# Kernel tuning notes

Measured on AMD Instinct MI355X. Metric: run time of the kernel, lower is better.

## Reference

```python
import jax, jax.numpy as jnp
import numpy as np
jax.config.update("jax_enable_x64", True)

MS_H = 10
MS_W = 10
EPS = 1e-8


def _window_mean(x, kh, kw):
    # x: [B, H, W]; VALID avg-pool with kernel (kh, kw), stride 1, via integral image
    c = jnp.cumsum(jnp.cumsum(x, axis=1), axis=2)
    c = jnp.pad(c, ((0, 0), (1, 0), (1, 0)))
    H, W = x.shape[1], x.shape[2]
    oh, ow = H - kh + 1, W - kw + 1
    s = (c[:, kh:kh + oh, kw:kw + ow] - c[:, :oh, kw:kw + ow]
         - c[:, kh:kh + oh, :ow] + c[:, :oh, :ow])
    return s / (kh * kw)


def _translate_bilinear(imgs, dy, dx):
    # imgs: [B, H, W]; out[b,i,j] = imgs[b, i - dy[b], j - dx[b]] (bilinear, zero fill)
    B, H, W = imgs.shape
    yq = jnp.arange(H, dtype=imgs.dtype)[None, :, None] - dy[:, None, None]
    xq = jnp.arange(W, dtype=imgs.dtype)[None, None, :] - dx[:, None, None]
    y0 = jnp.floor(yq); x0 = jnp.floor(xq)
    wy = yq - y0;       wx = xq - x0
    y0i = y0.astype(jnp.int32); x0i = x0.astype(jnp.int32)
    b = jnp.arange(B)[:, None, None]
    def samp(yi, xi):
        valid = (yi >= 0) & (yi < H) & (xi >= 0) & (xi < W)
        v = imgs[b, jnp.clip(yi, 0, H - 1), jnp.clip(xi, 0, W - 1)]
        return jnp.where(valid, v, jnp.zeros((), imgs.dtype))
    v00 = samp(y0i, x0i);     v01 = samp(y0i, x0i + 1)
    v10 = samp(y0i + 1, x0i); v11 = samp(y0i + 1, x0i + 1)
    return (v00 * (1 - wy) * (1 - wx) + v01 * (1 - wy) * wx
            + v10 * wy * (1 - wx) + v11 * wy * wx)


def _motion_correct(fr, template):
    # fr: [1, B, H, W, 1] float32; template: [H, W] float32
    B = fr.shape[1]
    H, W = template.shape
    mx, my = H // 2, W // 2
    # --- template normalization ---
    t_zm = template - jnp.mean(template)
    t_var = jnp.sum(jnp.square(t_zm)) + EPS
    target_freq = jnp.fft.fft2(t_zm.astype(jnp.complex128))            # [H, W]
    imgs = fr[0, :, :, :, 0]                                           # [B, H, W]
    imgs_zm = imgs - jnp.mean(imgs, axis=(1, 2), keepdims=True)
    # --- local statistics (avg_pool2d VALID, kernel = template minus shift margins) ---
    kh, kw = H - 2 * MS_W, W - 2 * MS_H
    m1 = _window_mean(imgs, kh, kw)                                    # [B, 2mw+1, 2mh+1]
    m2 = _window_mean(jnp.square(imgs), kh, kw)
    imgs_var = m2 - jnp.square(m1) / (kh * kw) + EPS
    imgs_var = jnp.where(imgs_var < 0, 0.0, imgs_var)
    denominator = jnp.sqrt(t_var * imgs_var)
    # --- FFT cross-correlation (fft3d over batch+spatial, exactly as the TF code) ---
    fr_freq = jnp.fft.fftn(imgs_zm.astype(jnp.complex128), axes=(0, 1, 2))
    img_product = fr_freq * jnp.conj(target_freq)[None]
    cc = jnp.abs(jnp.fft.ifftn(img_product, axes=(0, 1, 2))).astype(jnp.float32)
    rolled = jnp.roll(cc, (B, mx, my), axis=(0, 1, 2))
    nom = rolled[:, mx - MS_W:mx + MS_W + 1, my - MS_H:my + MS_H + 1]
    ncc = nom / denominator
    ncc = jnp.where(jnp.isnan(ncc), 0.0, ncc)                          # [B, 2mw+1, 2mh+1]
    # --- integer peak ---
    flat = ncc.reshape(B, -1)
    am = jnp.argmax(flat, axis=1)
    shx = am // (2 * MS_H + 1)
    shy = am % (2 * MS_H + 1)
    sh_x_n = -(shx - MS_H).astype(jnp.float32)
    sh_y_n = -(shy - MS_W).astype(jnp.float32)
    # --- log-parabolic sub-pixel refinement ---
    l = jnp.log(ncc)
    b = jnp.arange(B)
    lxm1 = l[b, shx - 1, shy]; lxp1 = l[b, shx + 1, shy]
    lym1 = l[b, shx, shy - 1]; lyp1 = l[b, shx, shy + 1]
    lc4 = 4.0 * l[b, shx, shy]
    sh_x_n = sh_x_n - (lxm1 - lxp1) / (2 * lxm1 - lc4 + 2 * lxp1)
    sh_y_n = sh_y_n - (lym1 - lyp1) / (2 * lym1 - lc4 + 2 * lyp1)
    # --- bilinear translate; tfa translations = [sh_y (dx, width), sh_x (dy, height)] ---
    warped = _translate_bilinear(imgs, sh_x_n, sh_y_n)                 # [B, H, W]
    return jnp.transpose(warped, (0, 2, 1)).reshape(B, H * W)


def setup_inputs() -> dict:
    H = W = 512
    B = 32
    k1, k2, k3 = jax.random.split(jax.random.key(0), 3)
    # smooth (low-pass) random template so the NCC peak is smooth/positive around its max
    noise = jax.random.normal(k1, (H, W))
    f = jnp.sqrt(jnp.fft.fftfreq(H)[:, None] ** 2 + jnp.fft.fftfreq(W)[None, :] ** 2)
    lp = (f < 0.05).astype(jnp.complex128)
    template = jnp.real(jnp.fft.ifft2(jnp.fft.fft2(noise) * lp))
    template = (template / template.std()).astype(jnp.float32)
    # frames: template shifted by small random integer offsets + noise
    shifts = jax.random.randint(k2, (B, 2), -5, 6)
    frames = jax.vmap(lambda s: jnp.roll(template, (s[0], s[1]), axis=(0, 1)))(shifts)
    frames = frames + 0.05 * jax.random.normal(k3, (B, H, W), dtype=jnp.float32)
    fr = frames[None, :, :, :, None].astype(jnp.float32)
    return {"fr": fr, "template": template}


def reference(fr, template):
    return _motion_correct(fr, template)
```

## Files before the change

kernel.cpp:

```cpp
#include <hip/hip_runtime.h>
#include <math.h>

#define HH 512
#define WW 512
#define NPIX (HH*WW)
#define NB 32
#define NS 21
#define KWIN 492
#define NKB 256
#define MT28 28
#define PARTSZ (MT28*32*16)

typedef __attribute__((ext_vector_type(8))) short short8;
typedef __attribute__((ext_vector_type(8))) unsigned short ushort8;
typedef __attribute__((ext_vector_type(4))) float floatx4;

__device__ __forceinline__ unsigned short f2bf(float f) {
    unsigned u = __float_as_uint(f);
    unsigned r = (u + 0x7fffu + ((u >> 16) & 1u)) >> 16;
    return (unsigned short)r;
}

__global__ __launch_bounds__(256) void stage1(
    const float* __restrict__ fr, const float* __restrict__ tpl,
    unsigned short* __restrict__ frBi, unsigned short* __restrict__ tplv,
    float* __restrict__ I1, float* __restrict__ I2,
    double* __restrict__ sum1, double* __restrict__ sum2)
{
    __shared__ unsigned short tile[64][136];
    int blk = blockIdx.x;
    int t   = threadIdx.x;
    if (blk < 512) {
        int kbase   = blk * 512;
        int kc8base = blk * 64;
        int sub  = t >> 7;
        int tq   = t & 127;
        int kc8l = tq >> 1;
        int j4   = (tq & 1) * 4;
#pragma unroll
        for (int h = 0; h < 2; ++h) {
#pragma unroll
            for (int n2 = 0; n2 < 16; n2 += 2) {
                int nl = n2 + sub;
                const float* src = fr + (size_t)(h * 16 + nl) * NPIX + kbase + tq * 4;
                float4 v = *(const float4*)src;
                unsigned short* d = &tile[kc8l][nl * 8 + j4];
                d[0] = f2bf(v.x); d[1] = f2bf(v.y); d[2] = f2bf(v.z); d[3] = f2bf(v.w);
            }
            __syncthreads();
            for (int c = t; c < 1024; c += 256) {
                int kl = c >> 4;
                int nl = c & 15;
                ushort8 o = *(ushort8*)&tile[kl][nl * 8];
                *(ushort8*)(frBi + ((size_t)(kc8base + kl) * 32 + h * 16 + nl) * 8) = o;
            }
            __syncthreads();
        }
    } else if (blk < 1024) {
        int id = blk - 512;
        int b  = id >> 4;
        int yg = id & 15;
        int y0, ny;
        if (yg < 8) { y0 = 20 + 30 * yg; ny = 30; }
        else        { y0 = 260 + 29 * (yg - 8); ny = 29; }
        const float* img = fr + (size_t)b * NPIX;
        int xa = t, xb = t + 256;
        float s1a = 0.f, s2a = 0.f, s1b = 0.f, s2b = 0.f;
        for (int y = y0; y < y0 + ny; ++y) {
            float va = img[(size_t)y * WW + xa];
            float vb = img[(size_t)y * WW + xb];
            s1a += va; s2a += va * va;
            s1b += vb; s2b += vb * vb;
        }
        atomicAdd(&I1[b * WW + xa], s1a); atomicAdd(&I2[b * WW + xa], s2a);
        atomicAdd(&I1[b * WW + xb], s1b); atomicAdd(&I2[b * WW + xb], s2b);
    } else if (blk < 1032) {
        int gq = blk - 1024;
        int y0 = 64 * gq;
        int xa = t, xb = t + 256;
        float s1a = 0.f, s2a = 0.f, s1b = 0.f, s2b = 0.f;
        for (int y = y0; y < y0 + 64; ++y) {
            float va = tpl[(size_t)y * WW + xa];
            float vb = tpl[(size_t)y * WW + xb];
            s1a += va; s2a += va * va;
            s1b += vb; s2b += vb * vb;
        }
        double d1 = (double)s1a + (double)s1b;
        double d2 = (double)s2a + (double)s2b;
        for (int off = 32; off; off >>= 1) {
            d1 += __shfl_down(d1, off);
            d2 += __shfl_down(d2, off);
        }
        __shared__ double r1[4], r2[4];
        int lane = t & 63, wv = t >> 6;
        if (lane == 0) { r1[wv] = d1; r2[wv] = d2; }
        __syncthreads();
        if (t == 0) {
            atomicAdd(&sum1[32], r1[0] + r1[1] + r1[2] + r1[3]);
            atomicAdd(&sum2[32], r2[0] + r2[1] + r2[2] + r2[3]);
        }
    } else {
        int blk2 = blk - 1032;
        int dv   = blk2 / 34;
        int prg  = blk2 % 34;
        int prEnd = min(16 * prg + 16, 532);
        for (int pr = 16 * prg; pr < prEnd; ++pr) {
            int sy = (pr + 502) & 511;
            const float* srow = tpl + (size_t)sy * WW;
            unsigned short* drow = tplv + ((size_t)dv * 532 + pr) * 512;
            for (int x = t; x < 512; x += 256) {
                int sx = (x - dv + 522) & 511;
                drow[x] = f2bf(srow[sx]);
            }
        }
    }
}

__global__ __launch_bounds__(448) void corr_mfma(
    const unsigned short* __restrict__ frBi,
    const unsigned short* __restrict__ tplv,
    float* __restrict__ part)
{
    const int l    = threadIdx.x & 63;
    const int mg2  = threadIdx.x >> 6;
    const int half = blockIdx.x & 1;
    const int idx  = blockIdx.x >> 1;
    const int kb   = ((idx & 7) << 5) | (idx >> 3);
    const int k0   = kb << 10;
    const int kg   = l >> 4;
    const int ln   = l & 15;
    const int tp   = 7 * half + mg2;

    const unsigned short* pA[2];
#pragma unroll
    for (int mt = 0; mt < 2; ++mt) {
        int m_g = 32 * tp + 16 * mt + ln;
        int du  = (m_g * 1561) >> 15;
        int dv  = m_g - 21 * du;
        if (m_g >= 441) { du = 0; dv = 0; }
        pA[mt] = tplv + ((size_t)(dv * 532 + 20 - du) * 512 + 8 * kg + k0);
    }
    const unsigned short* pB0 = frBi + ((size_t)k0 * 32 + kg * 256 + ln * 8);
    const unsigned short* pB1 = pB0 + 128;

    floatx4 acc00 = {}, acc01 = {}, acc10 = {}, acc11 = {};

#pragma unroll
    for (int ks = 0; ks < 32; ++ks) {
        short8 A0 = *(const short8*)pA[0];
        short8 A1 = *(const short8*)pA[1];
        short8 B0 = *(const short8*)pB0;
        short8 B1 = *(const short8*)pB1;
        acc00 = __builtin_amdgcn_mfma_f32_16x16x32_bf16(A0, B0, acc00, 0, 0, 0);
        acc01 = __builtin_amdgcn_mfma_f32_16x16x32_bf16(A0, B1, acc01, 0, 0, 0);
        acc10 = __builtin_amdgcn_mfma_f32_16x16x32_bf16(A1, B0, acc10, 0, 0, 0);
        acc11 = __builtin_amdgcn_mfma_f32_16x16x32_bf16(A1, B1, acc11, 0, 0, 0);
        pA[0] += 32; pA[1] += 32; pB0 += 1024; pB1 += 1024;
    }

    {
        size_t base = ((size_t)kb * MT28 + 2 * tp) * 32;
        floatx4* p;
        p = (floatx4*)(part + (base + ln)      * 16 + 4 * kg); *p = acc00;
        p = (floatx4*)(part + (base + 16 + ln) * 16 + 4 * kg); *p = acc01;
        p = (floatx4*)(part + (base + 32 + ln) * 16 + 4 * kg); *p = acc10;
        p = (floatx4*)(part + (base + 48 + ln) * 16 + 4 * kg); *p = acc11;
    }
}

__global__ __launch_bounds__(512) void reduce_stage2(
    const float* __restrict__ part, float* __restrict__ cc,
    const float* __restrict__ fr, const float* __restrict__ I1,
    const float* __restrict__ I2, double* __restrict__ sum1,
    const double* __restrict__ sum2, float* __restrict__ denom)
{
    __shared__ double wr1[NS][8], wr2[NS][8], wrT[8];
    __shared__ float  e1[NS][40], e2[NS][40];
    __shared__ double totals1[NS], totals2[NS];

    int blk = blockIdx.x;
    if (blk < 224) {
        int oct = blk / 28;
        int j   = (blk % 28) * 512 + threadIdx.x;
        const float* p = part + (size_t)(oct * 32) * PARTSZ + j;
        float s = 0.f;
#pragma unroll 8
        for (int i = 0; i < 32; ++i)
            s += p[(size_t)i * PARTSZ];
        int mr    = j & 15;
        int n     = (j >> 4) & 31;
        int mtile = j >> 9;
        int m = mtile * 16 + mr;
        if (m < 441)
            atomicAdd(&cc[(size_t)n * 441 + m], s);
        return;
    }

    int b = blk - 224;
    int x = threadIdx.x;
    const float* img = fr + (size_t)b * NPIX;
    float top[20], bot[20];
#pragma unroll
    for (int y = 0; y < 20; ++y) top[y] = img[(size_t)y * WW + x];
#pragma unroll
    for (int y = 0; y < 20; ++y) bot[y] = img[(size_t)(492 + y) * WW + x];

    float t1 = 0.f, t2 = 0.f, b1 = 0.f, b2 = 0.f;
#pragma unroll
    for (int y = 0; y < 20; ++y) {
        t1 += top[y]; t2 += top[y] * top[y];
        b1 += bot[y]; b2 += bot[y] * bot[y];
    }
    float i1 = I1[b * WW + x], i2 = I2[b * WW + x];
    int lane = x & 63, wv = x >> 6;

    double tot = (double)i1 + (double)t1 + (double)b1;
    for (int off = 32; off; off >>= 1) tot += __shfl_down(tot, off);
    if (lane == 0) wrT[wv] = tot;

    float s1 = i1 + t1, s2 = i2 + t2;
#pragma unroll
    for (int u = 0; u < NS; ++u) {
        if (u) {
            float a = top[u-1], c = bot[u-1];
            s1 += c - a;
            s2 += c * c - a * a;
        }
        double d1 = (double)s1, d2 = (double)s2;
        for (int off = 32; off; off >>= 1) {
            d1 += __shfl_down(d1, off);
            d2 += __shfl_down(d2, off);
        }
        if (lane == 0) { wr1[u][wv] = d1; wr2[u][wv] = d2; }
        if (x < 20)        { e1[u][x]       = s1; e2[u][x]       = s2; }
        else if (x >= 492) { e1[u][x - 472] = s1; e2[u][x - 472] = s2; }
    }
    __syncthreads();
    if (x == 0) {
        double s = 0.0;
        for (int i = 0; i < 8; ++i) s += wrT[i];
        sum1[b] = s;
    }
    if (x < NS) {
        double a = 0.0, c = 0.0;
        for (int i = 0; i < 8; ++i) { a += wr1[x][i]; c += wr2[x][i]; }
        totals1[x] = a; totals2[x] = c;
    }
    __syncthreads();
    if (x < NS * NS) {
        int u = x / NS, v = x - NS * u;
        double S1 = totals1[u], S2 = totals2[u];
        for (int j = 0; j < v; ++j)  { S1 -= (double)e1[u][j];      S2 -= (double)e2[u][j]; }
        for (int j = v; j < 20; ++j) { S1 -= (double)e1[u][20 + j]; S2 -= (double)e2[u][20 + j]; }
        const double inv = 1.0 / ((double)KWIN * (double)KWIN);
        double m1 = S1 * inv, m2 = S2 * inv;
        double var = m2 - (m1 * m1) * inv + 1e-8;
        if (var < 0.0) var = 0.0;
        double tv = sum2[32] - sum1[32] * sum1[32] * (1.0 / (double)NPIX) + 1e-8;
        denom[(size_t)b * NS * NS + x] = (float)sqrt(tv * var);
    }
}

__global__ __launch_bounds__(64) void argmax_kernel(
    const float* __restrict__ cc, const float* __restrict__ denom,
    const double* __restrict__ sum1, float* __restrict__ shifts)
{
    int b = blockIdx.x;
    const float* C = cc    + (size_t)b * NS * NS;
    const float* D = denom + (size_t)b * NS * NS;
    float corr = (float)(sum1[b] * sum1[32] * (1.0 / (double)NPIX));
    int l = threadIdx.x;
    float best = -1e30f; int bidx = NS * NS;
    for (int i = l; i < NS * NS; i += 64) {
        float v = fabsf(C[i] - corr) / D[i];
        if (v != v) v = 0.f;
        if (v > best) { best = v; bidx = i; }
    }
    for (int off = 32; off; off >>= 1) {
        float ov = __shfl_down(best, off);
        int   oi = __shfl_down(bidx, off);
        if (ov > best || (ov == best && oi < bidx)) { best = ov; bidx = oi; }
    }
    if (l == 0) {
        int shx = bidx / NS, shy = bidx % NS;
        auto nccAt = [&](int i, int j) -> float {
            i = (i < 0) ? i + NS : i; i = (i > NS - 1) ? NS - 1 : i;
            j = (j < 0) ? j + NS : j; j = (j > NS - 1) ? NS - 1 : j;
            float v = fabsf(C[i * NS + j] - corr) / D[i * NS + j];
            if (v != v) v = 0.f;
            return v;
        };
        float lc  = logf(nccAt(shx, shy));
        float lxm = logf(nccAt(shx - 1, shy));
        float lxp = logf(nccAt(shx + 1, shy));
        float lym = logf(nccAt(shx, shy - 1));
        float lyp = logf(nccAt(shx, shy + 1));
        float shxn = -(float)(shx - 10) - (lxm - lxp) / (2.f * lxm - 4.f * lc + 2.f * lxp);
        float shyn = -(float)(shy - 10) - (lym - lyp) / (2.f * lym - 4.f * lc + 2.f * lyp);
        shifts[b]      = shxn;
        shifts[32 + b] = shyn;
    }
}

__device__ __forceinline__ float samp(const float* __restrict__ img, int y, int x) {
    bool valid = (y >= 0) & (y < HH) & (x >= 0) & (x < WW);
    int yc = min(max(y, 0), HH - 1), xc = min(max(x, 0), WW - 1);
    float v = img[(size_t)yc * WW + xc];
    return valid ? v : 0.f;
}

__global__ __launch_bounds__(256) void warp_kernel(
    const float* __restrict__ fr, const float* __restrict__ shifts,
    float* __restrict__ out)
{
    int b  = blockIdx.z;
    int h0 = blockIdx.y * 32;
    int w0 = blockIdx.x * 32;
    float dy = shifts[b], dx = shifts[32 + b];
    const float* img = fr + (size_t)b * NPIX;
    __shared__ float tile[32][33];
    int tx = threadIdx.x & 31;
    int tz = threadIdx.x >> 5;
#pragma unroll
    for (int s = 0; s < 4; ++s) {
        int h = h0 + tz + 8 * s;
        int w = w0 + tx;
        float yq = (float)h - dy;
        float xq = (float)w - dx;
        float y0f = floorf(yq), x0f = floorf(xq);
        float wy = yq - y0f, wx = xq - x0f;
        int y0 = (int)y0f, x0 = (int)x0f;
        float v00 = samp(img, y0,     x0);
        float v01 = samp(img, y0,     x0 + 1);
        float v10 = samp(img, y0 + 1, x0);
        float v11 = samp(img, y0 + 1, x0 + 1);
        float val = v00 * (1.f - wy) * (1.f - wx) + v01 * (1.f - wy) * wx
                  + v10 * wy * (1.f - wx)         + v11 * wy * wx;
        tile[tz + 8 * s][tx] = val;
    }
    __syncthreads();
#pragma unroll
    for (int s = 0; s < 4; ++s) {
        int hh = tx;
        int ww = tz + 8 * s;
        out[(size_t)b * NPIX + (size_t)(w0 + ww) * HH + (h0 + hh)] = tile[hh][ww];
    }
}

extern "C" void kernel_launch(void* const* d_in, const int* in_sizes, int n_in,
                              void* d_out, int out_size, void* d_ws, size_t ws_size,
                              hipStream_t stream) {
    const float* fr  = (const float*)d_in[0];
    const float* tpl = (const float*)d_in[1];
    float* out = (float*)d_out;
    char* ws = (char*)d_ws;

    double* sum1    = (double*)(ws + 0);
    double* sum2    = (double*)(ws + 512);
    float*  cc      = (float*) (ws + 4096);
    float*  I1      = (float*) (ws + 61440);
    float*  I2      = (float*) (ws + 126976);
    float*  shifts  = (float*) (ws + 196608);
    float*  denom   = (float*) (ws + 200704);
    unsigned short* frBi = (unsigned short*)(ws + 262144);
    unsigned short* tplv = (unsigned short*)(ws + 17039360);
    float*  part    = (float*) (ws + 28508160);

    hipMemsetAsync(ws, 0, 192512, stream);

    stage1       <<<1746, 256, 0, stream>>>(fr, tpl, frBi, tplv, I1, I2, sum1, sum2);
    corr_mfma    <<<512, 448, 0, stream>>>(frBi, tplv, part);
    reduce_stage2<<<256, 512, 0, stream>>>(part, cc, fr, I1, I2, sum1, sum2, denom);
    argmax_kernel<<<32, 64, 0, stream>>>(cc, denom, sum1, shifts);
    warp_kernel  <<<dim3(16, 16, 32), 256, 0, stream>>>(fr, shifts, out);
}
```

Baseline: 163.4 us.

## Split correlation K into finer blocks, stage B in LDS, fuse argmax into warp

The correlation GEMM now uses 512 K-blocks of 512 instead of 256 of 1024, which doubles the grid. Each block stages its frame B-tile into shared memory, so the seven waves share one copy instead of each reading it from global memory. The reduction now sums 64 partials per output. The separate argmax kernel is removed, and every warp-kernel block recomputes the subpixel shift itself, trading one launch for redundant per-block argmax work (8192 blocks each scanning 441 values) and a larger partial buffer.

Measured after the change: 165.4 us. Within noise of the previous version (+1.2%).

```diff
diff --git a/kernel.cpp b/kernel.cpp
--- a/kernel.cpp
+++ b/kernel.cpp
@@ -7,7 +7,7 @@
 #define NB 32
 #define NS 21
 #define KWIN 492
-#define NKB 256
+#define NKB 512
 #define MT28 28
 #define PARTSZ (MT28*32*16)
 
@@ -121,41 +121,57 @@
     const unsigned short* __restrict__ tplv,
     float* __restrict__ part)
 {
+    __shared__ unsigned short Bs[16384];
+
     const int l    = threadIdx.x & 63;
     const int mg2  = threadIdx.x >> 6;
-    const int half = blockIdx.x & 1;
-    const int idx  = blockIdx.x >> 1;
-    const int kb   = ((idx & 7) << 5) | (idx >> 3);
-    const int k0   = kb << 10;
+    const int idx  = blockIdx.x & 511;
+    const int half = blockIdx.x >> 9;
+    const int kb   = ((idx & 7) << 6) | (idx >> 3);
+    const int k0   = kb << 9;
     const int kg   = l >> 4;
     const int ln   = l & 15;
     const int tp   = 7 * half + mg2;
 
-    const unsigned short* pA[2];
-#pragma unroll
-    for (int mt = 0; mt < 2; ++mt) {
-        int m_g = 32 * tp + 16 * mt + ln;
+    {
+        const ushort8* src = (const ushort8*)(frBi + (size_t)k0 * 32);
+        ushort8* dst = (ushort8*)Bs;
+        for (int i = threadIdx.x; i < 2048; i += 448)
+            dst[i] = src[i];
+    }
+
+    const unsigned short* pA0;
+    const unsigned short* pA1;
+    {
+        int m_g = 32 * tp + ln;
         int du  = (m_g * 1561) >> 15;
         int dv  = m_g - 21 * du;
         if (m_g >= 441) { du = 0; dv = 0; }
-        pA[mt] = tplv + ((size_t)(dv * 532 + 20 - du) * 512 + 8 * kg + k0);
-    }
-    const unsigned short* pB0 = frBi + ((size_t)k0 * 32 + kg * 256 + ln * 8);
-    const unsigned short* pB1 = pB0 + 128;
+        pA0 = tplv + ((size_t)(dv * 532 + 20 - du) * 512 + 8 * kg + k0);
+        m_g = 32 * tp + 16 + ln;
+        du  = (m_g * 1561) >> 15;
+        dv  = m_g - 21 * du;
+        if (m_g >= 441) { du = 0; dv = 0; }
+        pA1 = tplv + ((size_t)(dv * 532 + 20 - du) * 512 + 8 * kg + k0);
+    }
+
+    const unsigned short* lB = Bs + kg * 256 + ln * 8;
+
+    __syncthreads();
 
     floatx4 acc00 = {}, acc01 = {}, acc10 = {}, acc11 = {};
 
 #pragma unroll
-    for (int ks = 0; ks < 32; ++ks) {
-        short8 A0 = *(const short8*)pA[0];
-        short8 A1 = *(const short8*)pA[1];
-        short8 B0 = *(const short8*)pB0;
-        short8 B1 = *(const short8*)pB1;
+    for (int ks = 0; ks < 16; ++ks) {
+        short8 A0 = *(const short8*)pA0;
+        short8 A1 = *(const short8*)pA1;
+        short8 B0 = *(const short8*)(lB + ks * 1024);
+        short8 B1 = *(const short8*)(lB + ks * 1024 + 128);
         acc00 = __builtin_amdgcn_mfma_f32_16x16x32_bf16(A0, B0, acc00, 0, 0, 0);
         acc01 = __builtin_amdgcn_mfma_f32_16x16x32_bf16(A0, B1, acc01, 0, 0, 0);
         acc10 = __builtin_amdgcn_mfma_f32_16x16x32_bf16(A1, B0, acc10, 0, 0, 0);
         acc11 = __builtin_amdgcn_mfma_f32_16x16x32_bf16(A1, B1, acc11, 0, 0, 0);
-        pA[0] += 32; pA[1] += 32; pB0 += 1024; pB1 += 1024;
+        pA0 += 32; pA1 += 32;
     }
 
     {
@@ -182,10 +198,10 @@
     if (blk < 224) {
         int oct = blk / 28;
         int j   = (blk % 28) * 512 + threadIdx.x;
-        const float* p = part + (size_t)(oct * 32) * PARTSZ + j;
+        const float* p = part + (size_t)(oct * 64) * PARTSZ + j;
         float s = 0.f;
 #pragma unroll 8
-        for (int i = 0; i < 32; ++i)
+        for (int i = 0; i < 64; ++i)
             s += p[(size_t)i * PARTSZ];
         int mr    = j & 15;
         int n     = (j >> 4) & 31;
@@ -261,47 +277,6 @@
     }
 }
 
-__global__ __launch_bounds__(64) void argmax_kernel(
-    const float* __restrict__ cc, const float* __restrict__ denom,
-    const double* __restrict__ sum1, float* __restrict__ shifts)
-{
-    int b = blockIdx.x;
-    const float* C = cc    + (size_t)b * NS * NS;
-    const float* D = denom + (size_t)b * NS * NS;
-    float corr = (float)(sum1[b] * sum1[32] * (1.0 / (double)NPIX));
-    int l = threadIdx.x;
-    float best = -1e30f; int bidx = NS * NS;
-    for (int i = l; i < NS * NS; i += 64) {
-        float v = fabsf(C[i] - corr) / D[i];
-        if (v != v) v = 0.f;
-        if (v > best) { best = v; bidx = i; }
-    }
-    for (int off = 32; off; off >>= 1) {
-        float ov = __shfl_down(best, off);
-        int   oi = __shfl_down(bidx, off);
-        if (ov > best || (ov == best && oi < bidx)) { best = ov; bidx = oi; }
-    }
-    if (l == 0) {
-        int shx = bidx / NS, shy = bidx % NS;
-        auto nccAt = [&](int i, int j) -> float {
-            i = (i < 0) ? i + NS : i; i = (i > NS - 1) ? NS - 1 : i;
-            j = (j < 0) ? j + NS : j; j = (j > NS - 1) ? NS - 1 : j;
-            float v = fabsf(C[i * NS + j] - corr) / D[i * NS + j];
-            if (v != v) v = 0.f;
-            return v;
-        };
-        float lc  = logf(nccAt(shx, shy));
-        float lxm = logf(nccAt(shx - 1, shy));
-        float lxp = logf(nccAt(shx + 1, shy));
-        float lym = logf(nccAt(shx, shy - 1));
-        float lyp = logf(nccAt(shx, shy + 1));
-        float shxn = -(float)(shx - 10) - (lxm - lxp) / (2.f * lxm - 4.f * lc + 2.f * lxp);
-        float shyn = -(float)(shy - 10) - (lym - lyp) / (2.f * lym - 4.f * lc + 2.f * lyp);
-        shifts[b]      = shxn;
-        shifts[32 + b] = shyn;
-    }
-}
-
 __device__ __forceinline__ float samp(const float* __restrict__ img, int y, int x) {
     bool valid = (y >= 0) & (y < HH) & (x >= 0) & (x < WW);
     int yc = min(max(y, 0), HH - 1), xc = min(max(x, 0), WW - 1);
@@ -310,13 +285,63 @@
 }
 
 __global__ __launch_bounds__(256) void warp_kernel(
-    const float* __restrict__ fr, const float* __restrict__ shifts,
+    const float* __restrict__ fr, const float* __restrict__ cc,
+    const float* __restrict__ denom, const double* __restrict__ sum1,
     float* __restrict__ out)
 {
+    __shared__ float sdy, sdx;
+    __shared__ float wbest[4];
+    __shared__ int   wbidx[4];
+
     int b  = blockIdx.z;
+    int t  = threadIdx.x;
+
+    {
+        const float* C = cc    + (size_t)b * NS * NS;
+        const float* D = denom + (size_t)b * NS * NS;
+        float corr = (float)(sum1[b] * sum1[32] * (1.0 / (double)NPIX));
+        float best = -1e30f; int bidx = NS * NS;
+        for (int i = t; i < NS * NS; i += 256) {
+            float v = fabsf(C[i] - corr) / D[i];
+            if (v != v) v = 0.f;
+            if (v > best) { best = v; bidx = i; }
+        }
+        for (int off = 32; off; off >>= 1) {
+            float ov = __shfl_down(best, off);
+            int   oi = __shfl_down(bidx, off);
+            if (ov > best || (ov == best && oi < bidx)) { best = ov; bidx = oi; }
+        }
+        int lane = t & 63, wv = t >> 6;
+        if (lane == 0) { wbest[wv] = best; wbidx[wv] = bidx; }
+        __syncthreads();
+        if (t == 0) {
+            for (int i = 1; i < 4; ++i) {
+                if (wbest[i] > best || (wbest[i] == best && wbidx[i] < bidx)) {
+                    best = wbest[i]; bidx = wbidx[i];
+                }
+            }
+            int shx = bidx / NS, shy = bidx % NS;
+            auto nccAt = [&](int i, int j) -> float {
+                i = (i < 0) ? i + NS : i; i = (i > NS - 1) ? NS - 1 : i;
+                j = (j < 0) ? j + NS : j; j = (j > NS - 1) ? NS - 1 : j;
+                float v = fabsf(C[i * NS + j] - corr) / D[i * NS + j];
+                if (v != v) v = 0.f;
+                return v;
+            };
+            float lc  = logf(nccAt(shx, shy));
+            float lxm = logf(nccAt(shx - 1, shy));
+            float lxp = logf(nccAt(shx + 1, shy));
+            float lym = logf(nccAt(shx, shy - 1));
+            float lyp = logf(nccAt(shx, shy + 1));
+            sdy = -(float)(shx - 10) - (lxm - lxp) / (2.f * lxm - 4.f * lc + 2.f * lxp);
+            sdx = -(float)(shy - 10) - (lym - lyp) / (2.f * lym - 4.f * lc + 2.f * lyp);
+        }
+        __syncthreads();
+    }
+
+    float dy = sdy, dx = sdx;
     int h0 = blockIdx.y * 32;
     int w0 = blockIdx.x * 32;
-    float dy = shifts[b], dx = shifts[32 + b];
     const float* img = fr + (size_t)b * NPIX;
     __shared__ float tile[32][33];
     int tx = threadIdx.x & 31;
@@ -360,7 +385,6 @@
     float*  cc      = (float*) (ws + 4096);
     float*  I1      = (float*) (ws + 61440);
     float*  I2      = (float*) (ws + 126976);
-    float*  shifts  = (float*) (ws + 196608);
     float*  denom   = (float*) (ws + 200704);
     unsigned short* frBi = (unsigned short*)(ws + 262144);
     unsigned short* tplv = (unsigned short*)(ws + 17039360);
@@ -369,8 +393,7 @@
     hipMemsetAsync(ws, 0, 192512, stream);
 
     stage1       <<<1746, 256, 0, stream>>>(fr, tpl, frBi, tplv, I1, I2, sum1, sum2);
-    corr_mfma    <<<512, 448, 0, stream>>>(frBi, tplv, part);
+    corr_mfma    <<<1024, 448, 0, stream>>>(frBi, tplv, part);
     reduce_stage2<<<256, 512, 0, stream>>>(part, cc, fr, I1, I2, sum1, sum2, denom);
-    argmax_kernel<<<32, 64, 0, stream>>>(cc, denom, sum1, shifts);
-    warp_kernel  <<<dim3(16, 16, 32), 256, 0, stream>>>(fr, shifts, out);
-}
+    warp_kernel  <<<dim3(16, 16, 32), 256, 0, stream>>>(fr, cc, denom, sum1, out);
+}
```

## Fuse frame bf16 conversion into correlation kernel via shared-memory B tile

Applied to the files above, without the earlier changes.

Removes the separate frame-to-bf16 interleave pass from stage1 and instead has each correlation block load its 512-element K slice of all 32 frames, convert to bf16 and stage it in LDS. The correlation kernel now uses 14 waves per block covering all 441 shifts with half the K depth per block, doubling the number of K partials that the reduction sums. This avoids writing and re-reading the 16 MB intermediate frBi buffer, but doubles the partial-sum traffic and makes each block wait at a barrier for the LDS fill. The template-view write is also vectorised to ushort2 stores.

Measured after the change: 167.1 us. 1.02x slower.

```diff
diff --git a/kernel.cpp b/kernel.cpp
--- a/kernel.cpp
+++ b/kernel.cpp
@@ -7,7 +7,7 @@
 #define NB 32
 #define NS 21
 #define KWIN 492
-#define NKB 256
+#define NKB 512
 #define MT28 28
 #define PARTSZ (MT28*32*16)
 
@@ -23,41 +23,14 @@
 
 __global__ __launch_bounds__(256) void stage1(
     const float* __restrict__ fr, const float* __restrict__ tpl,
-    unsigned short* __restrict__ frBi, unsigned short* __restrict__ tplv,
+    unsigned short* __restrict__ tplv,
     float* __restrict__ I1, float* __restrict__ I2,
     double* __restrict__ sum1, double* __restrict__ sum2)
 {
-    __shared__ unsigned short tile[64][136];
     int blk = blockIdx.x;
     int t   = threadIdx.x;
     if (blk < 512) {
-        int kbase   = blk * 512;
-        int kc8base = blk * 64;
-        int sub  = t >> 7;
-        int tq   = t & 127;
-        int kc8l = tq >> 1;
-        int j4   = (tq & 1) * 4;
-#pragma unroll
-        for (int h = 0; h < 2; ++h) {
-#pragma unroll
-            for (int n2 = 0; n2 < 16; n2 += 2) {
-                int nl = n2 + sub;
-                const float* src = fr + (size_t)(h * 16 + nl) * NPIX + kbase + tq * 4;
-                float4 v = *(const float4*)src;
-                unsigned short* d = &tile[kc8l][nl * 8 + j4];
-                d[0] = f2bf(v.x); d[1] = f2bf(v.y); d[2] = f2bf(v.z); d[3] = f2bf(v.w);
-            }
-            __syncthreads();
-            for (int c = t; c < 1024; c += 256) {
-                int kl = c >> 4;
-                int nl = c & 15;
-                ushort8 o = *(ushort8*)&tile[kl][nl * 8];
-                *(ushort8*)(frBi + ((size_t)(kc8base + kl) * 32 + h * 16 + nl) * 8) = o;
-            }
-            __syncthreads();
-        }
-    } else if (blk < 1024) {
-        int id = blk - 512;
+        int id = blk;
         int b  = id >> 4;
         int yg = id & 15;
         int y0, ny;
@@ -74,8 +47,8 @@
         }
         atomicAdd(&I1[b * WW + xa], s1a); atomicAdd(&I2[b * WW + xa], s2a);
         atomicAdd(&I1[b * WW + xb], s1b); atomicAdd(&I2[b * WW + xb], s2b);
-    } else if (blk < 1032) {
-        int gq = blk - 1024;
+    } else if (blk < 520) {
+        int gq = blk - 512;
         int y0 = 64 * gq;
         int xa = t, xb = t + 256;
         float s1a = 0.f, s2a = 0.f, s1b = 0.f, s2b = 0.f;
@@ -100,66 +73,87 @@
             atomicAdd(&sum2[32], r2[0] + r2[1] + r2[2] + r2[3]);
         }
     } else {
-        int blk2 = blk - 1032;
+        int blk2 = blk - 520;
         int dv   = blk2 / 34;
         int prg  = blk2 % 34;
         int prEnd = min(16 * prg + 16, 532);
+        int x2 = 2 * t;
         for (int pr = 16 * prg; pr < prEnd; ++pr) {
             int sy = (pr + 502) & 511;
             const float* srow = tpl + (size_t)sy * WW;
             unsigned short* drow = tplv + ((size_t)dv * 532 + pr) * 512;
-            for (int x = t; x < 512; x += 256) {
-                int sx = (x - dv + 522) & 511;
-                drow[x] = f2bf(srow[sx]);
-            }
-        }
-    }
-}
-
-__global__ __launch_bounds__(448) void corr_mfma(
-    const unsigned short* __restrict__ frBi,
+            int sx0 = (x2     - dv + 522) & 511;
+            int sx1 = (x2 + 1 - dv + 522) & 511;
+            ushort2 o;
+            o.x = f2bf(srow[sx0]);
+            o.y = f2bf(srow[sx1]);
+            *(ushort2*)(drow + x2) = o;
+        }
+    }
+}
+
+__global__ __launch_bounds__(896) void corr_mfma(
+    const float* __restrict__ fr,
     const unsigned short* __restrict__ tplv,
     float* __restrict__ part)
 {
-    const int l    = threadIdx.x & 63;
-    const int mg2  = threadIdx.x >> 6;
-    const int half = blockIdx.x & 1;
-    const int idx  = blockIdx.x >> 1;
-    const int kb   = ((idx & 7) << 5) | (idx >> 3);
-    const int k0   = kb << 10;
-    const int kg   = l >> 4;
-    const int ln   = l & 15;
-    const int tp   = 7 * half + mg2;
-
-    const unsigned short* pA[2];
-#pragma unroll
-    for (int mt = 0; mt < 2; ++mt) {
-        int m_g = 32 * tp + 16 * mt + ln;
+    __shared__ unsigned short Bs[16384];
+
+    const int t   = threadIdx.x;
+    const int l   = t & 63;
+    const int wid = t >> 6;
+    const int idx = blockIdx.x;
+    const int kb  = ((idx & 7) << 6) | (idx >> 3);
+    const int k0  = kb << 9;
+    const int kg  = l >> 4;
+    const int ln  = l & 15;
+
+    for (int i = t; i < 4096; i += 896) {
+        int frame = i >> 7;
+        int q     = i & 127;
+        float4 v = *(const float4*)(fr + (size_t)frame * NPIX + k0 + 4 * q);
+        int k8 = q >> 1, j4 = (q & 1) * 4;
+        ushort4 o;
+        o.x = f2bf(v.x); o.y = f2bf(v.y); o.z = f2bf(v.z); o.w = f2bf(v.w);
+        *(ushort4*)&Bs[(k8 * 32 + frame) * 8 + j4] = o;
+    }
+
+    const unsigned short* pA0;
+    const unsigned short* pA1;
+    {
+        int m_g = 32 * wid + ln;
         int du  = (m_g * 1561) >> 15;
         int dv  = m_g - 21 * du;
         if (m_g >= 441) { du = 0; dv = 0; }
-        pA[mt] = tplv + ((size_t)(dv * 532 + 20 - du) * 512 + 8 * kg + k0);
-    }
-    const unsigned short* pB0 = frBi + ((size_t)k0 * 32 + kg * 256 + ln * 8);
-    const unsigned short* pB1 = pB0 + 128;
+        pA0 = tplv + ((size_t)(dv * 532 + 20 - du) * 512 + 8 * kg + k0);
+        m_g = 32 * wid + 16 + ln;
+        du  = (m_g * 1561) >> 15;
+        dv  = m_g - 21 * du;
+        if (m_g >= 441) { du = 0; dv = 0; }
+        pA1 = tplv + ((size_t)(dv * 532 + 20 - du) * 512 + 8 * kg + k0);
+    }
+
+    const unsigned short* lB = Bs + kg * 256 + ln * 8;
+
+    __syncthreads();
 
     floatx4 acc00 = {}, acc01 = {}, acc10 = {}, acc11 = {};
 
 #pragma unroll
-    for (int ks = 0; ks < 32; ++ks) {
-        short8 A0 = *(const short8*)pA[0];
-        short8 A1 = *(const short8*)pA[1];
-        short8 B0 = *(const short8*)pB0;
-        short8 B1 = *(const short8*)pB1;
+    for (int ks = 0; ks < 16; ++ks) {
+        short8 A0 = *(const short8*)pA0;
+        short8 A1 = *(const short8*)pA1;
+        short8 B0 = *(const short8*)(lB + ks * 1024);
+        short8 B1 = *(const short8*)(lB + ks * 1024 + 128);
         acc00 = __builtin_amdgcn_mfma_f32_16x16x32_bf16(A0, B0, acc00, 0, 0, 0);
         acc01 = __builtin_amdgcn_mfma_f32_16x16x32_bf16(A0, B1, acc01, 0, 0, 0);
         acc10 = __builtin_amdgcn_mfma_f32_16x16x32_bf16(A1, B0, acc10, 0, 0, 0);
         acc11 = __builtin_amdgcn_mfma_f32_16x16x32_bf16(A1, B1, acc11, 0, 0, 0);
-        pA[0] += 32; pA[1] += 32; pB0 += 1024; pB1 += 1024;
+        pA0 += 32; pA1 += 32;
     }
 
     {
-        size_t base = ((size_t)kb * MT28 + 2 * tp) * 32;
+        size_t base = ((size_t)kb * MT28 + 2 * wid) * 32;
         floatx4* p;
         p = (floatx4*)(part + (base + ln)      * 16 + 4 * kg); *p = acc00;
         p = (floatx4*)(part + (base + 16 + ln) * 16 + 4 * kg); *p = acc01;
@@ -182,10 +176,10 @@
     if (blk < 224) {
         int oct = blk / 28;
         int j   = (blk % 28) * 512 + threadIdx.x;
-        const float* p = part + (size_t)(oct * 32) * PARTSZ + j;
+        const float* p = part + (size_t)(oct * 64) * PARTSZ + j;
         float s = 0.f;
 #pragma unroll 8
-        for (int i = 0; i < 32; ++i)
+        for (int i = 0; i < 64; ++i)
             s += p[(size_t)i * PARTSZ];
         int mr    = j & 15;
         int n     = (j >> 4) & 31;
@@ -362,14 +356,13 @@
     float*  I2      = (float*) (ws + 126976);
     float*  shifts  = (float*) (ws + 196608);
     float*  denom   = (float*) (ws + 200704);
-    unsigned short* frBi = (unsigned short*)(ws + 262144);
-    unsigned short* tplv = (unsigned short*)(ws + 17039360);
-    float*  part    = (float*) (ws + 28508160);
+    unsigned short* tplv = (unsigned short*)(ws + 262144);
+    float*  part    = (float*) (ws + 16777216);
 
     hipMemsetAsync(ws, 0, 192512, stream);
 
-    stage1       <<<1746, 256, 0, stream>>>(fr, tpl, frBi, tplv, I1, I2, sum1, sum2);
-    corr_mfma    <<<512, 448, 0, stream>>>(frBi, tplv, part);
+    stage1       <<<1234, 256, 0, stream>>>(fr, tpl, tplv, I1, I2, sum1, sum2);
+    corr_mfma    <<<512, 896, 0, stream>>>(fr, tplv, part);
     reduce_stage2<<<256, 512, 0, stream>>>(part, cc, fr, I1, I2, sum1, sum2, denom);
     argmax_kernel<<<32, 64, 0, stream>>>(cc, denom, sum1, shifts);
     warp_kernel  <<<dim3(16, 16, 32), 256, 0, stream>>>(fr, shifts, out);
```
